# Kernel optimization log

Hardware: AMD Instinct MI355X
Metric: run time of the kernel (lower is better)

## Reference

```python
import jax, jax.numpy as jnp
import numpy as np

TEMPERATURE = 0.5
EPS = 1e-12  # matches torch F.normalize default eps


def setup_inputs() -> dict:
    key = jax.random.key(0)
    k1, k2 = jax.random.split(key)
    proj_1 = jax.random.normal(k1, (4096, 128), dtype=jnp.float32)
    proj_2 = jax.random.normal(k2, (4096, 128), dtype=jnp.float32)
    return {"proj_1": proj_1, "proj_2": proj_2}


def _l2_normalize(x):
    # torch F.normalize(p=2): x / max(||x||, eps)
    norm = jnp.linalg.norm(x, axis=1, keepdims=True)
    return x / jnp.maximum(norm, EPS)


def reference(proj_1, proj_2):
    n = proj_1.shape[0]
    z_i = _l2_normalize(proj_1)
    z_j = _l2_normalize(proj_2)
    reps = jnp.concatenate([z_i, z_j], axis=0)            # [2N, D]
    # cosine similarity of normalized vectors == dot product
    sim = reps @ reps.T                                    # [2N, 2N]
    sim_ij = jnp.diagonal(sim, offset=n)                   # [N]
    sim_ji = jnp.diagonal(sim, offset=-n)                  # [N]
    positives = jnp.concatenate([sim_ij, sim_ji], axis=0)  # [2N]
    nominator = jnp.exp(positives / TEMPERATURE)
    mask = 1.0 - jnp.eye(2 * n, dtype=sim.dtype)           # zero out self-similarity
    denominator = jnp.sum(mask * jnp.exp(sim / TEMPERATURE), axis=1)  # [2N]
    all_losses = -jnp.log(nominator / denominator)
    loss = jnp.sum(all_losses) / (2 * n)
    return loss
```

## Files before the change

### kernel.cpp

```cpp
#include <hip/hip_runtime.h>
#include <stdint.h>

typedef __bf16 bf16;
typedef bf16 bf16x8 __attribute__((ext_vector_type(8)));
typedef float floatx4 __attribute__((ext_vector_type(4)));

#define INV_T     2.0f
#define SQRT_K    1.6986436206f
#define INV_K     0.34657359028f
#define GLOBAL_AS __attribute__((address_space(1)))
#define LDS_AS    __attribute__((address_space(3)))


__global__ __launch_bounds__(256) void nrm_kernel(const float* __restrict__ p1,
                                                  const float* __restrict__ p2,
                                                  uint32_t* __restrict__ rep2,
                                                  float* __restrict__ out) {
    int gt   = blockIdx.x * 256 + threadIdx.x;
    int row  = gt >> 6;
    int lane = gt & 63;
    const float* srcRow = (row < 4096) ? (p1 + (size_t)row * 128)
                                       : (p2 + (size_t)(row - 4096) * 128);
    float2 v = ((const float2*)srcRow)[lane];
    float ss = v.x * v.x + v.y * v.y;
#pragma unroll
    for (int s = 1; s < 64; s <<= 1) ss += __shfl_xor(ss, s, 64);
    float inv = SQRT_K / fmaxf(sqrtf(ss), 1e-12f);
    union { bf16 h[2]; uint32_t u; } pk;
    pk.h[0] = (bf16)(v.x * inv);
    pk.h[1] = (bf16)(v.y * inv);
    int chunk = (row >> 6) * 1024 + (lane >> 2) * 64 + (row & 63);
    rep2[chunk * 4 + (lane & 3)] = pk.u;
    if (gt == 0) *out = 0.0f;
}

__global__ __launch_bounds__(256, 3) void sim_kernel(const uint4* __restrict__ rep2,
                                                     float* __restrict__ rowsumP,
                                                     float* __restrict__ pos) {
    __shared__ uint4 lB[2][1024];

    const int cc   = blockIdx.x;
    const int rb   = blockIdx.y;
    const int tid  = threadIdx.x;
    const int w    = tid >> 6;
    const int lane = tid & 63;
    const int quad = lane >> 4;
    const int lcol = lane & 15;

    const int wbase = rb * 256 + w * 64;
    const int pbase = (wbase + 4096) & 8191;

    bf16x8 aF[4][4];
    const uint4* aG = rep2 + (size_t)(wbase >> 6) * 1024;
#pragma unroll
    for (int mi = 0; mi < 4; mi++)
#pragma unroll
        for (int ks = 0; ks < 4; ks++)
            aF[mi][ks] = *(const bf16x8*)&aG[(ks * 4 + quad) * 64 + mi * 16 + lcol];

    float rs[16];
#pragma unroll
    for (int i = 0; i < 16; i++) rs[i] = 0.0f;

    {
        const uint4* src = rep2 + (size_t)(cc * 4) * 1024;
#pragma unroll
        for (int j = 0; j < 4; j++)
            __builtin_amdgcn_global_load_lds(
                (const GLOBAL_AS uint32_t*)(src + j * 256 + tid),
                (LDS_AS uint32_t*)&lB[0][j * 256 + tid], 16, 0, 0);
    }
    __syncthreads();

    for (int t = 0; t < 4; t++) {
        const int cur = t & 1;
        if (t < 3) {
            const uint4* src = rep2 + (size_t)(cc * 4 + t + 1) * 1024;
#pragma unroll
            for (int j = 0; j < 4; j++)
                __builtin_amdgcn_global_load_lds(
                    (const GLOBAL_AS uint32_t*)(src + j * 256 + tid),
                    (LDS_AS uint32_t*)&lB[cur ^ 1][j * 256 + tid], 16, 0, 0);
        }

        const int c0t = cc * 256 + t * 64;
#pragma unroll
        for (int so = 0; so < 4; so++) {
            bf16x8 bF[4];
#pragma unroll
            for (int ks = 0; ks < 4; ks++)
                bF[ks] = *(const bf16x8*)&lB[cur][(ks * 4 + quad) * 64 + so * 16 + lcol];

            floatx4 acc[4];
            const floatx4 zf = {0.0f, 0.0f, 0.0f, 0.0f};
#pragma unroll
            for (int mi = 0; mi < 4; mi++) acc[mi] = zf;
#pragma unroll
            for (int ks = 0; ks < 4; ks++)
#pragma unroll
                for (int mi = 0; mi < 4; mi++)
                    acc[mi] = __builtin_amdgcn_mfma_f32_16x16x32_bf16(
                        aF[mi][ks], bF[ks], acc[mi], 0, 0, 0);

            const int c0s  = c0t + so * 16;
            const int gcol = c0s + lcol;
            const bool diagS = ((c0s & ~63) == wbase);
            const bool partS = ((c0s & ~63) == pbase);
            if (diagS | partS) {
#pragma unroll
                for (int mi = 0; mi < 4; mi++)
#pragma unroll
                    for (int r = 0; r < 4; r++) {
                        int grow = wbase + mi * 16 + quad * 4 + r;
                        float s = acc[mi][r];
                        if (partS && gcol == ((grow + 4096) & 8191))
                            pos[grow] = s * INV_K;
                        float e = __builtin_amdgcn_exp2f(s);
                        if (diagS && grow == gcol) e = 0.0f;
                        rs[mi * 4 + r] += e;
                    }
            } else {
#pragma unroll
                for (int mi = 0; mi < 4; mi++)
#pragma unroll
                    for (int r = 0; r < 4; r++)
                        rs[mi * 4 + r] += __builtin_amdgcn_exp2f(acc[mi][r]);
            }
        }
        __syncthreads();
    }

#pragma unroll
    for (int s = 1; s < 16; s <<= 1)
#pragma unroll
        for (int k = 0; k < 16; k++) rs[k] += __shfl_xor(rs[k], s, 64);

    if (lcol == 0) {
#pragma unroll
        for (int k = 0; k < 16; k++) {
            int grow = wbase + (k >> 2) * 16 + quad * 4 + (k & 3);
            rowsumP[(size_t)grow * 32 + cc] = rs[k];
        }
    }
}

__global__ __launch_bounds__(128) void fin_kernel(const float* __restrict__ rowsumP,
                                                  const float* __restrict__ pos,
                                                  float* __restrict__ out) {
    int row = blockIdx.x * 128 + threadIdx.x;
    const floatx4* rp = (const floatx4*)(rowsumP + (size_t)row * 32);
    float d = 0.0f;
#pragma unroll
    for (int j = 0; j < 8; j++) {
        floatx4 q = rp[j];
        d += (q[0] + q[1]) + (q[2] + q[3]);
    }
    float v = logf(d) - pos[row] * INV_T;
#pragma unroll
    for (int s = 1; s < 64; s <<= 1) v += __shfl_xor(v, s, 64);
    __shared__ float red[2];
    if ((threadIdx.x & 63) == 0) red[threadIdx.x >> 6] = v;
    __syncthreads();
    if (threadIdx.x == 0)
        atomicAdd(out, (red[0] + red[1]) * (1.0f / 8192.0f));
}

extern "C" void kernel_launch(void* const* d_in, const int* in_sizes, int n_in,
                              void* d_out, int out_size, void* d_ws, size_t ws_size,
                              hipStream_t stream) {
    const float* p1 = (const float*)d_in[0];
    const float* p2 = (const float*)d_in[1];
    float* out = (float*)d_out;

    char* ws       = (char*)d_ws;
    uint32_t* rep2 = (uint32_t*)ws;
    float* rowsumP = (float*)(ws + (2u << 20));
    float* pos     = (float*)(ws + (3u << 20));

    nrm_kernel<<<2048, 256, 0, stream>>>(p1, p2, rep2, out);
    sim_kernel<<<dim3(32, 32), 256, 0, stream>>>((const uint4*)rep2, rowsumP, pos);
    fin_kernel<<<64, 128, 0, stream>>>(rowsumP, pos, out);
}
```

Measured before the change: 91.25 us.

## Exploit similarity matrix symmetry by computing only upper-triangular block tiles

After: 139.8 us. 53.2% more time.

```diff
diff --git a/kernel.cpp b/kernel.cpp
--- a/kernel.cpp
+++ b/kernel.cpp
@@ -34,13 +34,16 @@
     if (gt == 0) *out = 0.0f;
 }
 
-__global__ __launch_bounds__(256, 3) void sim_kernel(const uint4* __restrict__ rep2,
+__global__ __launch_bounds__(256, 4) void sim_kernel(const uint4* __restrict__ rep2,
                                                      float* __restrict__ rowsumP,
                                                      float* __restrict__ pos) {
     __shared__ uint4 lB[2][1024];
-
-    const int cc   = blockIdx.x;
-    const int rb   = blockIdx.y;
+    __shared__ float colPart[4][256];
+
+    const int cb = blockIdx.x;
+    const int rb = blockIdx.y;
+    if (cb < rb) return;
+
     const int tid  = threadIdx.x;
     const int w    = tid >> 6;
     const int lane = tid & 63;
@@ -63,7 +66,7 @@
     for (int i = 0; i < 16; i++) rs[i] = 0.0f;
 
     {
-        const uint4* src = rep2 + (size_t)(cc * 4) * 1024;
+        const uint4* src = rep2 + (size_t)(cb * 4) * 1024;
 #pragma unroll
         for (int j = 0; j < 4; j++)
             __builtin_amdgcn_global_load_lds(
@@ -75,7 +78,7 @@
     for (int t = 0; t < 4; t++) {
         const int cur = t & 1;
         if (t < 3) {
-            const uint4* src = rep2 + (size_t)(cc * 4 + t + 1) * 1024;
+            const uint4* src = rep2 + (size_t)(cb * 4 + t + 1) * 1024;
 #pragma unroll
             for (int j = 0; j < 4; j++)
                 __builtin_amdgcn_global_load_lds(
@@ -83,7 +86,6 @@
                     (LDS_AS uint32_t*)&lB[cur ^ 1][j * 256 + tid], 16, 0, 0);
         }
 
-        const int c0t = cc * 256 + t * 64;
 #pragma unroll
         for (int so = 0; so < 4; so++) {
             bf16x8 bF[4];
@@ -102,10 +104,11 @@
                     acc[mi] = __builtin_amdgcn_mfma_f32_16x16x32_bf16(
                         aF[mi][ks], bF[ks], acc[mi], 0, 0, 0);
 
-            const int c0s  = c0t + so * 16;
+            const int c0s  = cb * 256 + t * 64 + so * 16;
             const int gcol = c0s + lcol;
             const bool diagS = ((c0s & ~63) == wbase);
             const bool partS = ((c0s & ~63) == pbase);
+            float cs = 0.0f;
             if (diagS | partS) {
 #pragma unroll
                 for (int mi = 0; mi < 4; mi++)
@@ -113,19 +116,29 @@
                     for (int r = 0; r < 4; r++) {
                         int grow = wbase + mi * 16 + quad * 4 + r;
                         float s = acc[mi][r];
-                        if (partS && gcol == ((grow + 4096) & 8191))
-                            pos[grow] = s * INV_K;
+                        if (partS && gcol == grow + 4096) {
+                            float d = s * INV_K;
+                            pos[grow] = d;
+                            pos[grow + 4096] = d;
+                        }
                         float e = __builtin_amdgcn_exp2f(s);
                         if (diagS && grow == gcol) e = 0.0f;
                         rs[mi * 4 + r] += e;
+                        cs += e;
                     }
             } else {
 #pragma unroll
                 for (int mi = 0; mi < 4; mi++)
 #pragma unroll
-                    for (int r = 0; r < 4; r++)
-                        rs[mi * 4 + r] += __builtin_amdgcn_exp2f(acc[mi][r]);
+                    for (int r = 0; r < 4; r++) {
+                        float e = __builtin_amdgcn_exp2f(acc[mi][r]);
+                        rs[mi * 4 + r] += e;
+                        cs += e;
+                    }
             }
+            cs += __shfl_xor(cs, 16, 64);
+            cs += __shfl_xor(cs, 32, 64);
+            if (quad == 0) colPart[w][t * 64 + so * 16 + lcol] = cs;
         }
         __syncthreads();
     }
@@ -139,8 +152,13 @@
 #pragma unroll
         for (int k = 0; k < 16; k++) {
             int grow = wbase + (k >> 2) * 16 + quad * 4 + (k & 3);
-            rowsumP[(size_t)grow * 32 + cc] = rs[k];
+            rowsumP[(size_t)grow * 32 + cb] = rs[k];
         }
+    }
+
+    if (rb != cb) {
+        float c = colPart[0][tid] + colPart[1][tid] + colPart[2][tid] + colPart[3][tid];
+        rowsumP[(size_t)(cb * 256 + tid) * 32 + rb] = c;
     }
 }
 
```
